# Kernel optimization log

Hardware: AMD Instinct MI355X
Metric: run time of the kernel (lower is better)

## Reference

```python
import jax, jax.numpy as jnp
import numpy as np

N_NODES = 50000
N_EDGES = 800000
IN_DIM = 128
HID = 8
HEADS = 8
OUT_DIM = 64
NEG_SLOPE = 0.2


def setup_inputs() -> dict:
    key = jax.random.key(0)
    ks = jax.random.split(key, 8)
    x = jax.random.normal(ks[0], (N_NODES, IN_DIM), dtype=jnp.float32)
    edge_index = jax.random.randint(ks[1], (2, N_EDGES), 0, N_NODES, dtype=jnp.int64)
    W1 = jax.random.normal(ks[2], (IN_DIM, HEADS * HID), dtype=jnp.float32) / np.sqrt(IN_DIM)
    a_src1 = jax.random.normal(ks[3], (HEADS, HID), dtype=jnp.float32)
    a_dst1 = jax.random.normal(ks[4], (HEADS, HID), dtype=jnp.float32)
    b1 = jnp.zeros((HEADS * HID,), dtype=jnp.float32)
    W2 = jax.random.normal(ks[5], (HEADS * HID, OUT_DIM), dtype=jnp.float32) / np.sqrt(HEADS * HID)
    a_src2 = jax.random.normal(ks[6], (1, OUT_DIM), dtype=jnp.float32)
    a_dst2 = jax.random.normal(ks[7], (1, OUT_DIM), dtype=jnp.float32)
    b2 = jnp.zeros((OUT_DIM,), dtype=jnp.float32)
    return {"x": x, "edge_index": edge_index, "W1": W1, "a_src1": a_src1,
            "a_dst1": a_dst1, "b1": b1, "W2": W2, "a_src2": a_src2,
            "a_dst2": a_dst2, "b2": b2}


def gat_conv(x, src, dst, W, a_src, a_dst, b, heads, ch):
    # PyG GATConv (eval mode): linear -> per-edge LeakyReLU score ->
    # segment-softmax over incoming edges -> weighted scatter-add -> +bias
    n = x.shape[0]
    h = (x @ W).reshape(n, heads, ch)               # [N,H,C]
    score_src = jnp.einsum('nhc,hc->nh', h, a_src)  # [N,H]
    score_dst = jnp.einsum('nhc,hc->nh', h, a_dst)  # [N,H]
    e = jax.nn.leaky_relu(score_src[src] + score_dst[dst], NEG_SLOPE)  # [E,H]
    m = jax.ops.segment_max(e, dst, num_segments=n)
    m = jnp.where(jnp.isfinite(m), m, 0.0)
    p = jnp.exp(e - m[dst])
    denom = jax.ops.segment_sum(p, dst, num_segments=n)
    alpha = p / (denom[dst] + 1e-16)                # [E,H]
    out = jax.ops.segment_sum(h[src] * alpha[:, :, None], dst, num_segments=n)
    return out.reshape(n, heads * ch) + b


def reference(x, edge_index, W1, a_src1, a_dst1, b1, W2, a_src2, a_dst2, b2):
    n = x.shape[0]
    # add_self_loops=True (PyG default)
    loops = jnp.arange(n, dtype=edge_index.dtype)
    src = jnp.concatenate([edge_index[0], loops])
    dst = jnp.concatenate([edge_index[1], loops])
    h = gat_conv(x, src, dst, W1, a_src1, a_dst1, b1, HEADS, HID)
    h = jax.nn.elu(h)
    out = gat_conv(h, src, dst, W2, a_src2, a_dst2, b2, 1, OUT_DIM)
    return out
```

## Files before the change

### kernel.cpp

```cpp
#include <hip/hip_runtime.h>
#include <hip/hip_fp16.h>
#include <math.h>

#define N_NODES 50000
#define N_EDGES 800000
#define ET (N_EDGES + N_NODES)
#define IN_DIM 128
#define H1DIM 64
#define HEADS 8
#define HID 8
#define OUT_DIM 64
#define NEG_SLOPE 0.2f

#define SCAN_TILE 256
#define NTILES ((N_NODES + SCAN_TILE - 1) / SCAN_TILE)
#define RC 8
#define PF 6

#define LIN1_WAVES (N_NODES / 16)
#define LIN1_BLOCKS ((LIN1_WAVES + 3) / 4)
#define EB ((ET + 255) / 256)

typedef _Float16 half8 __attribute__((ext_vector_type(8)));
typedef float f32x4 __attribute__((ext_vector_type(4)));

__device__ __forceinline__ float lrelu(float v) { return v >= 0.f ? v : NEG_SLOPE * v; }

__device__ __forceinline__ int xcc_id() {
    int v;
    asm volatile("s_getreg_b32 %0, hwreg(HW_REG_XCC_ID)" : "=s"(v));
    return v & 7;
}

__device__ __forceinline__ void fma8raw(uint4 u, float alpha, float* a) {
    float2 f0 = __half22float2(*(const __half2*)&u.x);
    float2 f1 = __half22float2(*(const __half2*)&u.y);
    float2 f2 = __half22float2(*(const __half2*)&u.z);
    float2 f3 = __half22float2(*(const __half2*)&u.w);
    a[0] += f0.x * alpha; a[1] += f0.y * alpha;
    a[2] += f1.x * alpha; a[3] += f1.y * alpha;
    a[4] += f2.x * alpha; a[5] += f2.y * alpha;
    a[6] += f3.x * alpha; a[7] += f3.y * alpha;
}

__device__ __forceinline__ void fma8h(const __half* __restrict__ base, float alpha, float* a) {
    fma8raw(*reinterpret_cast<const uint4*>(base), alpha, a);
}

__device__ __forceinline__ void edge_nodes(const int* __restrict__ ei, int e, int& s, int& d) {
    if (e < N_EDGES) { s = ei[e]; d = ei[N_EDGES + e]; }
    else             { s = e - N_EDGES; d = s; }
}


__global__ __launch_bounds__(256) void cl1_kernel(
    const int* __restrict__ ei, int* __restrict__ cnt8, int* __restrict__ pos,
    const float* __restrict__ x, const float* __restrict__ W1,
    const float* __restrict__ a_src, const float* __restrict__ a_dst,
    __half* __restrict__ h1, float* __restrict__ ssrc, float* __restrict__ sdst)
{
    if (blockIdx.x >= LIN1_BLOCKS) {
        int i = (blockIdx.x - LIN1_BLOCKS) * 256 + threadIdx.x;
        if (i >= ET) return;
        int s, d; edge_nodes(ei, i, s, d);
        int c = xcc_id();
        int r = atomicAdd(&cnt8[c * N_NODES + d], 1);
        pos[i] = r | (c << 28);
        return;
    }

    __shared__ __half bH[16 * 512];
    __shared__ __half bL[16 * 512];

    int tid = threadIdx.x;
    #pragma unroll
    for (int i = 0; i < 32; ++i) {
        int idx = i * 256 + tid;
        int f = idx >> 9, rr = idx & 511;
        int l = rr >> 3, j = rr & 7;
        int ks = f >> 2, ct = f & 3;
        int k = ks * 32 + ((l >> 4) << 3) + j;
        int c = (ct << 4) + (l & 15);
        float w = W1[k * 64 + c];
        __half hi = __float2half(w);
        bH[idx] = hi;
        bL[idx] = __float2half(w - __half2float(hi));
    }
    __syncthreads();

    int wid = tid >> 6, t = tid & 63;
    int g = blockIdx.x * 4 + wid;
    if (g >= LIN1_WAVES) return;
    int n0 = g * 16;
    int row = t & 15, kq = t >> 4;

    f32x4 acc[4] = {};
    const float* xp = x + (size_t)(n0 + row) * IN_DIM + kq * 8;
    #pragma unroll
    for (int ks = 0; ks < 4; ++ks) {
        float4 u0 = *reinterpret_cast<const float4*>(xp + ks * 32);
        float4 u1 = *reinterpret_cast<const float4*>(xp + ks * 32 + 4);
        float xv[8] = {u0.x, u0.y, u0.z, u0.w, u1.x, u1.y, u1.z, u1.w};
        half8 ah, al;
        #pragma unroll
        for (int j = 0; j < 8; ++j) {
            _Float16 h = (_Float16)xv[j];
            ah[j] = h;
            al[j] = (_Float16)(xv[j] - (float)h);
        }
        #pragma unroll
        for (int ct = 0; ct < 4; ++ct) {
            int f = ks * 4 + ct;
            half8 bh = *reinterpret_cast<const half8*>(&bH[f * 512 + t * 8]);
            half8 bl = *reinterpret_cast<const half8*>(&bL[f * 512 + t * 8]);
            acc[ct] = __builtin_amdgcn_mfma_f32_16x16x32_f16(ah, bh, acc[ct], 0, 0, 0);
            acc[ct] = __builtin_amdgcn_mfma_f32_16x16x32_f16(al, bh, acc[ct], 0, 0, 0);
            acc[ct] = __builtin_amdgcn_mfma_f32_16x16x32_f16(ah, bl, acc[ct], 0, 0, 0);
        }
    }

    float asv[4], adv[4];
    #pragma unroll
    for (int ct = 0; ct < 4; ++ct) {
        asv[ct] = a_src[ct * 16 + (t & 15)];
        adv[ct] = a_dst[ct * 16 + (t & 15)];
    }
    int rbase = n0 + (t >> 4) * 4;
    #pragma unroll
    for (int r = 0; r < 4; ++r) {
        int n = rbase + r;
        #pragma unroll
        for (int ct = 0; ct < 4; ++ct) {
            float v = acc[ct][r];
            h1[(size_t)n * 64 + ct * 16 + (t & 15)] = __float2half(v);
            float ps = v * asv[ct], pd = v * adv[ct];
            ps += __shfl_xor(ps, 1); ps += __shfl_xor(ps, 2); ps += __shfl_xor(ps, 4);
            pd += __shfl_xor(pd, 1); pd += __shfl_xor(pd, 2); pd += __shfl_xor(pd, 4);
            if ((t & 7) == 0) {
                int hd = ct * 2 + ((t >> 3) & 1);
                ssrc[n * 8 + hd] = ps;
                sdst[n * 8 + hd] = pd;
            }
        }
    }
}


__global__ __launch_bounds__(SCAN_TILE) void scanA_kernel(
    const int* __restrict__ cnt8, int* __restrict__ row, int* __restrict__ aux)
{
    __shared__ int sh[SCAN_TILE];
    int t = threadIdx.x, i = blockIdx.x * SCAN_TILE + t;
    int v = 0;
    if (i < N_NODES) {
        #pragma unroll
        for (int c = 0; c < 8; ++c) v += cnt8[c * N_NODES + i];
    }
    sh[t] = v;
    __syncthreads();
    #pragma unroll
    for (int off = 1; off < SCAN_TILE; off <<= 1) {
        int add = (t >= off) ? sh[t - off] : 0;
        __syncthreads();
        sh[t] += add;
        __syncthreads();
    }
    if (i < N_NODES) row[i] = sh[t] - v;
    if (t == SCAN_TILE - 1) aux[blockIdx.x] = sh[t];
}

__global__ __launch_bounds__(SCAN_TILE) void scanB_kernel(int* __restrict__ aux, int* __restrict__ row) {
    __shared__ int sh[SCAN_TILE];
    int t = threadIdx.x;
    int v = (t < NTILES) ? aux[t] : 0;
    sh[t] = v;
    __syncthreads();
    #pragma unroll
    for (int off = 1; off < SCAN_TILE; off <<= 1) {
        int add = (t >= off) ? sh[t - off] : 0;
        __syncthreads();
        sh[t] += add;
        __syncthreads();
    }
    if (t < NTILES) aux[t] = sh[t] - v;
    if (t == NTILES - 1) row[N_NODES] = sh[t];
}

__global__ __launch_bounds__(SCAN_TILE) void scanC_kernel(
    const int* __restrict__ aux, int* __restrict__ row,
    const int* __restrict__ cnt8, int* __restrict__ off8)
{
    int i = blockIdx.x * SCAN_TILE + threadIdx.x;
    if (i >= N_NODES) return;
    int r = row[i] + aux[i >> 8];
    row[i] = r;
    int run = r;
    #pragma unroll
    for (int c = 0; c < 8; ++c) {
        off8[c * N_NODES + i] = run;
        run += cnt8[c * N_NODES + i];
    }
}

__global__ void fill_kernel(const int* __restrict__ ei, const int* __restrict__ off8,
                            const int* __restrict__ pos, int* __restrict__ adj)
{
    int i = blockIdx.x * blockDim.x + threadIdx.x;
    if (i >= ET) return;
    int s, d; edge_nodes(ei, i, s, d);
    int pr = pos[i];
    int c = (unsigned)pr >> 28;
    int r = pr & 0x0FFFFFFF;
    adj[off8[c * N_NODES + d] + r] = s;
}


__global__ __launch_bounds__(256) void l1_kernel(
    const int* __restrict__ row, const int* __restrict__ adj,
    const __half* __restrict__ h1, const float* __restrict__ s1, const float* __restrict__ t1,
    const float* __restrict__ b1, const float* __restrict__ W2,
    const float* __restrict__ as2, const float* __restrict__ ad2,
    __half* __restrict__ h2, float* __restrict__ s2, float* __restrict__ t2)
{
    int wid = threadIdx.x >> 6, t = threadIdx.x & 63;
    int half = t >> 5, tt = t & 31;
    int n = blockIdx.x * 8 + wid * 2 + half;
    int beg = row[n], end = row[n + 1];
    int slot = tt >> 3, h = tt & 7;
    float sd = t1[n * 8 + h];
    const int e0 = beg + slot;
    const int hb = half << 5;

    int   sv[RC];
    float p[RC];
    uint4 raw[PF];
    float m = -3e38f;
    #pragma unroll
    for (int it = 0; it < RC; ++it) {
        int e = e0 + it * 4;
        bool ok = e < end;
        int s = ok ? adj[e] : n;
        sv[it] = s;
        float v = ok ? lrelu(s1[s * 8 + h] + sd) : -3e38f;
        p[it] = v;
        m = fmaxf(m, v);
        if (it < PF) raw[it] = *reinterpret_cast<const uint4*>(h1 + (size_t)s * 64 + h * 8);
    }
    for (int e = e0 + RC * 4; e < end; e += 4)
        m = fmaxf(m, lrelu(s1[adj[e] * 8 + h] + sd));
    m = fmaxf(m, __shfl_xor(m, 8));
    m = fmaxf(m, __shfl_xor(m, 16));

    float den = 0.f;
    #pragma unroll
    for (int it = 0; it < RC; ++it) {
        float pe = __expf(p[it] - m);
        p[it] = pe;
        den += pe;
    }
    for (int e = e0 + RC * 4; e < end; e += 4)
        den += __expf(lrelu(s1[adj[e] * 8 + h] + sd) - m);
    den += __shfl_xor(den, 8);
    den += __shfl_xor(den, 16);
    float inv = 1.f / (den + 1e-16f);

    float a[8] = {0,0,0,0,0,0,0,0};
    #pragma unroll
    for (int it = 0; it < PF; ++it) fma8raw(raw[it], p[it] * inv, a);
    #pragma unroll
    for (int it = PF; it < RC; ++it) {
        int e = e0 + it * 4;
        if (e < end) fma8h(h1 + (size_t)sv[it] * 64 + h * 8, p[it] * inv, a);
    }
    for (int e = e0 + RC * 4; e < end; e += 4) {
        int s = adj[e];
        float alpha = __expf(lrelu(s1[s * 8 + h] + sd) - m) * inv;
        fma8h(h1 + (size_t)s * 64 + h * 8, alpha, a);
    }
    #pragma unroll
    for (int j = 0; j < 8; ++j) {
        a[j] += __shfl_xor(a[j], 8);
        a[j] += __shfl_xor(a[j], 16);
    }

    float ha0 = 0.f, ha1 = 0.f;
    int srcA = hb + (tt >> 3);
    #pragma unroll
    for (int j = 0; j < 8; ++j) {
        float vA = __shfl(a[j], srcA);
        float vB = __shfl(a[j], srcA + 4);
        if ((tt & 7) == j) { ha0 = vA; ha1 = vB; }
    }

    ha0 += b1[tt];
    ha1 += b1[tt + 32];
    ha0 = ha0 > 0.f ? ha0 : (__expf(ha0) - 1.f);
    ha1 = ha1 > 0.f ? ha1 : (__expf(ha1) - 1.f);

    float c0 = 0.f, c1 = 0.f;
    #pragma unroll 8
    for (int k = 0; k < 32; ++k) {
        float w = __shfl(ha0, hb + k);
        c0 += w * W2[k * 64 + tt];
        c1 += w * W2[k * 64 + tt + 32];
    }
    #pragma unroll 8
    for (int k = 0; k < 32; ++k) {
        float w = __shfl(ha1, hb + k);
        c0 += w * W2[(k + 32) * 64 + tt];
        c1 += w * W2[(k + 32) * 64 + tt + 32];
    }
    h2[n * 64 + tt]      = __float2half(c0);
    h2[n * 64 + tt + 32] = __float2half(c1);

    float rs = c0 * as2[tt] + c1 * as2[tt + 32];
    float rd = c0 * ad2[tt] + c1 * ad2[tt + 32];
    #pragma unroll
    for (int mk = 16; mk >= 1; mk >>= 1) {
        rs += __shfl_xor(rs, mk);
        rd += __shfl_xor(rd, mk);
    }
    if (tt == 0) { s2[n] = rs; t2[n] = rd; }
}


__global__ __launch_bounds__(256) void l2_kernel(
    const int* __restrict__ row, const int* __restrict__ adj,
    const __half* __restrict__ h2, const float* __restrict__ s2, const float* __restrict__ t2,
    const float* __restrict__ b2, float* __restrict__ out)
{
    int wid = threadIdx.x >> 6, t = threadIdx.x & 63;
    int half = t >> 5, tt = t & 31;
    int n = blockIdx.x * 8 + wid * 2 + half;
    int beg = row[n], end = row[n + 1];
    int slot = tt >> 3, g = tt & 7;
    float sd = t2[n];
    const int e0 = beg + slot;

    int   sv[RC];
    float p[RC];
    uint4 raw[PF];
    float m = -3e38f;
    #pragma unroll
    for (int it = 0; it < RC; ++it) {
        int e = e0 + it * 4;
        bool ok = e < end;
        int s = ok ? adj[e] : n;
        sv[it] = s;
        float v = ok ? lrelu(s2[s] + sd) : -3e38f;
        p[it] = v;
        m = fmaxf(m, v);
        if (it < PF) raw[it] = *reinterpret_cast<const uint4*>(h2 + (size_t)s * 64 + g * 8);
    }
    for (int e = e0 + RC * 4; e < end; e += 4)
        m = fmaxf(m, lrelu(s2[adj[e]] + sd));
    m = fmaxf(m, __shfl_xor(m, 8));
    m = fmaxf(m, __shfl_xor(m, 16));

    float den = 0.f;
    #pragma unroll
    for (int it = 0; it < RC; ++it) {
        float pe = __expf(p[it] - m);
        p[it] = pe;
        den += pe;
    }
    for (int e = e0 + RC * 4; e < end; e += 4)
        den += __expf(lrelu(s2[adj[e]] + sd) - m);
    den += __shfl_xor(den, 8);
    den += __shfl_xor(den, 16);
    float inv = 1.f / (den + 1e-16f);

    float a[8] = {0,0,0,0,0,0,0,0};
    #pragma unroll
    for (int it = 0; it < PF; ++it) fma8raw(raw[it], p[it] * inv, a);
    #pragma unroll
    for (int it = PF; it < RC; ++it) {
        int e = e0 + it * 4;
        if (e < end) fma8h(h2 + (size_t)sv[it] * 64 + g * 8, p[it] * inv, a);
    }
    for (int e = e0 + RC * 4; e < end; e += 4) {
        int s = adj[e];
        float alpha = __expf(lrelu(s2[s] + sd) - m) * inv;
        fma8h(h2 + (size_t)s * 64 + g * 8, alpha, a);
    }
    #pragma unroll
    for (int j = 0; j < 8; ++j) {
        a[j] += __shfl_xor(a[j], 8);
        a[j] += __shfl_xor(a[j], 16);
    }
    if (slot == 0) {
        float4 o0 = make_float4(a[0] + b2[g * 8 + 0], a[1] + b2[g * 8 + 1],
                                a[2] + b2[g * 8 + 2], a[3] + b2[g * 8 + 3]);
        float4 o1 = make_float4(a[4] + b2[g * 8 + 4], a[5] + b2[g * 8 + 5],
                                a[6] + b2[g * 8 + 6], a[7] + b2[g * 8 + 7]);
        float4* op = (float4*)(out + (size_t)n * 64 + g * 8);
        op[0] = o0; op[1] = o1;
    }
}

extern "C" void kernel_launch(void* const* d_in, const int* in_sizes, int n_in,
                              void* d_out, int out_size, void* d_ws, size_t ws_size,
                              hipStream_t stream)
{
    const float* x   = (const float*)d_in[0];
    const int* ei    = (const int*)d_in[1];
    const float* W1  = (const float*)d_in[2];
    const float* as1 = (const float*)d_in[3];
    const float* ad1 = (const float*)d_in[4];
    const float* b1  = (const float*)d_in[5];
    const float* W2  = (const float*)d_in[6];
    const float* as2 = (const float*)d_in[7];
    const float* ad2 = (const float*)d_in[8];
    const float* b2  = (const float*)d_in[9];
    float* out = (float*)d_out;

    char* wsb = (char*)d_ws;
    __half* h1  = (__half*)wsb;
    __half* h2  = h1 + (size_t)N_NODES * 64;
    float*  s1  = (float*)(h2 + (size_t)N_NODES * 64);
    float*  t1  = s1 + N_NODES * 8;
    float*  s2  = t1 + N_NODES * 8;
    float*  t2  = s2 + N_NODES;
    int*    cnt8 = (int*)(t2 + N_NODES);
    int*    off8 = cnt8 + 8 * N_NODES;
    int*    rowp = off8 + 8 * N_NODES;
    int*    aux  = rowp + N_NODES + 1;
    int*    adj  = aux + NTILES;
    int*    pos  = adj + ET;

    hipMemsetAsync(cnt8, 0, 8 * N_NODES * sizeof(int), stream);

    cl1_kernel<<<LIN1_BLOCKS + EB, 256, 0, stream>>>(ei, cnt8, pos, x, W1, as1, ad1, h1, s1, t1);

    scanA_kernel<<<NTILES, SCAN_TILE, 0, stream>>>(cnt8, rowp, aux);
    scanB_kernel<<<1, SCAN_TILE, 0, stream>>>(aux, rowp);
    scanC_kernel<<<NTILES, SCAN_TILE, 0, stream>>>(aux, rowp, cnt8, off8);
    fill_kernel<<<EB, 256, 0, stream>>>(ei, off8, pos, adj);

    l1_kernel<<<N_NODES / 8, 256, 0, stream>>>(rowp, adj, h1, s1, t1,
                                               b1, W2, as2, ad2, h2, s2, t2);

    l2_kernel<<<N_NODES / 8, 256, 0, stream>>>(rowp, adj, h2, s2, t2, b2, out);
}
```

Measured before the change: 221.4 us.

## Split layer-2 linear out of l1 into MFMA-based lin2 kernel

Layer-1 aggregation now writes the ELU-activated hidden features to a float workspace instead of computing the 64x64 projection with shuffle-based scalar FMAs inline. A new lin2 kernel performs that projection with fp16 MFMA using a split hi/lo scheme (three MFMAs per tile) to keep near-fp32 accuracy. It also computes the layer-2 attention scores. The aim is to take the shuffle-heavy dense matmul off the latency-bound gather kernel. In exchange it adds an extra kernel launch and a 12.8MB fp32 round trip through memory.

After: 215.2 us. -2.8%, faster.

```diff
diff --git a/kernel.cpp b/kernel.cpp
--- a/kernel.cpp
+++ b/kernel.cpp
@@ -1,6 +1,7 @@
 #include <hip/hip_runtime.h>
 #include <hip/hip_fp16.h>
 #include <math.h>
+#include <stdint.h>
 
 #define N_NODES 50000
 #define N_EDGES 800000
@@ -19,6 +20,8 @@
 
 #define LIN1_WAVES (N_NODES / 16)
 #define LIN1_BLOCKS ((LIN1_WAVES + 3) / 4)
+#define LIN2_WAVES (N_NODES / 16)
+#define LIN2_BLOCKS ((LIN2_WAVES + 3) / 4)
 #define EB ((ET + 255) / 256)
 
 typedef _Float16 half8 __attribute__((ext_vector_type(8)));
@@ -218,9 +221,7 @@
 __global__ __launch_bounds__(256) void l1_kernel(
     const int* __restrict__ row, const int* __restrict__ adj,
     const __half* __restrict__ h1, const float* __restrict__ s1, const float* __restrict__ t1,
-    const float* __restrict__ b1, const float* __restrict__ W2,
-    const float* __restrict__ as2, const float* __restrict__ ad2,
-    __half* __restrict__ h2, float* __restrict__ s2, float* __restrict__ t2)
+    const float* __restrict__ b1, float* __restrict__ ha)
 {
     int wid = threadIdx.x >> 6, t = threadIdx.x & 63;
     int half = t >> 5, tt = t & 31;
@@ -229,7 +230,6 @@
     int slot = tt >> 3, h = tt & 7;
     float sd = t1[n * 8 + h];
     const int e0 = beg + slot;
-    const int hb = half << 5;
 
     int   sv[RC];
     float p[RC];
@@ -283,44 +283,94 @@
         a[j] += __shfl_xor(a[j], 16);
     }
 
-    float ha0 = 0.f, ha1 = 0.f;
-    int srcA = hb + (tt >> 3);
-    #pragma unroll
-    for (int j = 0; j < 8; ++j) {
-        float vA = __shfl(a[j], srcA);
-        float vB = __shfl(a[j], srcA + 4);
-        if ((tt & 7) == j) { ha0 = vA; ha1 = vB; }
-    }
-
-    ha0 += b1[tt];
-    ha1 += b1[tt + 32];
-    ha0 = ha0 > 0.f ? ha0 : (__expf(ha0) - 1.f);
-    ha1 = ha1 > 0.f ? ha1 : (__expf(ha1) - 1.f);
-
-    float c0 = 0.f, c1 = 0.f;
-    #pragma unroll 8
-    for (int k = 0; k < 32; ++k) {
-        float w = __shfl(ha0, hb + k);
-        c0 += w * W2[k * 64 + tt];
-        c1 += w * W2[k * 64 + tt + 32];
-    }
-    #pragma unroll 8
-    for (int k = 0; k < 32; ++k) {
-        float w = __shfl(ha1, hb + k);
-        c0 += w * W2[(k + 32) * 64 + tt];
-        c1 += w * W2[(k + 32) * 64 + tt + 32];
-    }
-    h2[n * 64 + tt]      = __float2half(c0);
-    h2[n * 64 + tt + 32] = __float2half(c1);
-
-    float rs = c0 * as2[tt] + c1 * as2[tt + 32];
-    float rd = c0 * ad2[tt] + c1 * ad2[tt + 32];
-    #pragma unroll
-    for (int mk = 16; mk >= 1; mk >>= 1) {
-        rs += __shfl_xor(rs, mk);
-        rd += __shfl_xor(rd, mk);
-    }
-    if (tt == 0) { s2[n] = rs; t2[n] = rd; }
+    int j0 = slot * 2;
+    float v0 = a[j0]     + b1[h * 8 + j0];
+    float v1 = a[j0 + 1] + b1[h * 8 + j0 + 1];
+    v0 = v0 > 0.f ? v0 : (__expf(v0) - 1.f);
+    v1 = v1 > 0.f ? v1 : (__expf(v1) - 1.f);
+    *reinterpret_cast<float2*>(ha + (size_t)n * 64 + h * 8 + j0) = make_float2(v0, v1);
+}
+
+
+__global__ __launch_bounds__(256) void lin2_kernel(
+    const float* __restrict__ ha, const float* __restrict__ W2,
+    const float* __restrict__ as2, const float* __restrict__ ad2,
+    __half* __restrict__ h2, float* __restrict__ s2, float* __restrict__ t2)
+{
+    __shared__ __half bH[8 * 512];
+    __shared__ __half bL[8 * 512];
+
+    int tid = threadIdx.x;
+    #pragma unroll
+    for (int i = 0; i < 16; ++i) {
+        int idx = i * 256 + tid;
+        int f = idx >> 9, rr = idx & 511;
+        int l = rr >> 3, j = rr & 7;
+        int ks = f >> 2, ct = f & 3;
+        int k = ks * 32 + ((l >> 4) << 3) + j;
+        int c = (ct << 4) + (l & 15);
+        float w = W2[k * 64 + c];
+        __half hi = __float2half(w);
+        bH[idx] = hi;
+        bL[idx] = __float2half(w - __half2float(hi));
+    }
+    __syncthreads();
+
+    int wid = tid >> 6, t = tid & 63;
+    int g = blockIdx.x * 4 + wid;
+    if (g >= LIN2_WAVES) return;
+    int n0 = g * 16;
+    int row = t & 15, kq = t >> 4;
+
+    f32x4 acc[4] = {};
+    const float* xp = ha + (size_t)(n0 + row) * 64 + kq * 8;
+    #pragma unroll
+    for (int ks = 0; ks < 2; ++ks) {
+        float4 u0 = *reinterpret_cast<const float4*>(xp + ks * 32);
+        float4 u1 = *reinterpret_cast<const float4*>(xp + ks * 32 + 4);
+        float xv[8] = {u0.x, u0.y, u0.z, u0.w, u1.x, u1.y, u1.z, u1.w};
+        half8 ah, al;
+        #pragma unroll
+        for (int j = 0; j < 8; ++j) {
+            _Float16 hh = (_Float16)xv[j];
+            ah[j] = hh;
+            al[j] = (_Float16)(xv[j] - (float)hh);
+        }
+        #pragma unroll
+        for (int ct = 0; ct < 4; ++ct) {
+            int f = ks * 4 + ct;
+            half8 bh = *reinterpret_cast<const half8*>(&bH[f * 512 + t * 8]);
+            half8 bl = *reinterpret_cast<const half8*>(&bL[f * 512 + t * 8]);
+            acc[ct] = __builtin_amdgcn_mfma_f32_16x16x32_f16(ah, bh, acc[ct], 0, 0, 0);
+            acc[ct] = __builtin_amdgcn_mfma_f32_16x16x32_f16(al, bh, acc[ct], 0, 0, 0);
+            acc[ct] = __builtin_amdgcn_mfma_f32_16x16x32_f16(ah, bl, acc[ct], 0, 0, 0);
+        }
+    }
+
+    float asv[4], adv[4];
+    #pragma unroll
+    for (int ct = 0; ct < 4; ++ct) {
+        asv[ct] = as2[ct * 16 + (t & 15)];
+        adv[ct] = ad2[ct * 16 + (t & 15)];
+    }
+    int rbase = n0 + (t >> 4) * 4;
+    #pragma unroll
+    for (int r = 0; r < 4; ++r) {
+        int n = rbase + r;
+        float ps = 0.f, pd = 0.f;
+        #pragma unroll
+        for (int ct = 0; ct < 4; ++ct) {
+            float v = acc[ct][r];
+            h2[(size_t)n * 64 + ct * 16 + (t & 15)] = __float2half(v);
+            ps += v * asv[ct];
+            pd += v * adv[ct];
+        }
+        ps += __shfl_xor(ps, 1); ps += __shfl_xor(ps, 2);
+        ps += __shfl_xor(ps, 4); ps += __shfl_xor(ps, 8);
+        pd += __shfl_xor(pd, 1); pd += __shfl_xor(pd, 2);
+        pd += __shfl_xor(pd, 4); pd += __shfl_xor(pd, 8);
+        if ((t & 15) == 0) { s2[n] = ps; t2[n] = pd; }
+    }
 }
 
 
@@ -427,6 +477,7 @@
     int*    aux  = rowp + N_NODES + 1;
     int*    adj  = aux + NTILES;
     int*    pos  = adj + ET;
+    float*  ha   = (float*)(((uintptr_t)(pos + ET) + 15) & ~(uintptr_t)15);
 
     hipMemsetAsync(cnt8, 0, 8 * N_NODES * sizeof(int), stream);
 
@@ -437,8 +488,9 @@
     scanC_kernel<<<NTILES, SCAN_TILE, 0, stream>>>(aux, rowp, cnt8, off8);
     fill_kernel<<<EB, 256, 0, stream>>>(ei, off8, pos, adj);
 
-    l1_kernel<<<N_NODES / 8, 256, 0, stream>>>(rowp, adj, h1, s1, t1,
-                                               b1, W2, as2, ad2, h2, s2, t2);
+    l1_kernel<<<N_NODES / 8, 256, 0, stream>>>(rowp, adj, h1, s1, t1, b1, ha);
+
+    lin2_kernel<<<LIN2_BLOCKS, 256, 0, stream>>>(ha, W2, as2, ad2, h2, s2, t2);
 
     l2_kernel<<<N_NODES / 8, 256, 0, stream>>>(rowp, adj, h2, s2, t2, b2, out);
 }
```
